# Optimization experiments

Measured on AMD Instinct MI355X. Metric: run time of the kernel, lower is better.

## Reference

```python
import jax, jax.numpy as jnp
import numpy as np

N_TOKENS = 100000
UNITS = 150  # CustomizeLSTMCell.TRANSITION_STATE_OUTPUTS_DIM


def setup_inputs() -> dict:
    key = jax.random.key(0)
    ks = jax.random.split(key, 9)
    f = lambda k, shape: jax.random.normal(k, shape, dtype=jnp.float32)
    return {
        "s_in": f(ks[0], (N_TOKENS, UNITS)),
        "s_out": f(ks[1], (N_TOKENS, UNITS)),
        "h_in": f(ks[2], (N_TOKENS, UNITS)),
        "h_out": f(ks[3], (N_TOKENS, UNITS)),
        "last_c": f(ks[4], (N_TOKENS, UNITS)),
        "w_in_input": f(ks[5], (UNITS, UNITS)) * 0.05,
        "w_out_input": f(ks[6], (UNITS, UNITS)) * 0.05,
        "u_in_input": f(ks[7], (UNITS, UNITS)) * 0.05,
        "u_out_input": f(ks[8], (UNITS, UNITS)) * 0.05,
    }


def reference(s_in, s_out, h_in, h_out, last_c,
              w_in_input, w_out_input, u_in_input, u_out_input):
    # Faithful to the source: all four gates use the *_input weights and no bias
    # (the original call() computes identical pre-activations for every gate).
    pre = (s_in @ w_in_input + s_out @ w_out_input
           + h_in @ u_in_input + h_out @ u_out_input)  # [N, H]
    gate = jax.nn.sigmoid(pre)
    # input_gate == output_gate == forget_gate == update_gate == gate
    cell_state = gate * last_c + gate * gate
    hidden_state = gate * jnp.tanh(cell_state)
    return hidden_state, cell_state
```

## Files before the change

kernel.cpp:

```cpp
#include <hip/hip_runtime.h>
#include <hip/hip_bf16.h>

typedef __attribute__((ext_vector_type(8))) short short8;
typedef __attribute__((ext_vector_type(4))) float f32x4;

#define NTOK   100000
#define H      150
#define NKS    20
#define BM     64
#define SLAB   38400
#define NCHUNK 38
#define BUFB   (NCHUNK*1024)
#define OUTOFF (NTOK * H)
#define XLIM   ((long)NTOK * H * 4 - 16)

__device__ __forceinline__ unsigned short f2bf(float f) {
    unsigned int u = __builtin_bit_cast(unsigned int, f);
    u = (u + 0x7FFFu + ((u >> 16) & 1u)) >> 16;
    return (unsigned short)u;
}

__global__ void prep_w(const float* __restrict__ w_in, const float* __restrict__ w_out,
                       const float* __restrict__ u_in, const float* __restrict__ u_out,
                       unsigned short* __restrict__ wb) {
    int idx = blockIdx.x * 256 + threadIdx.x;
    if (idx >= 10 * NKS * 64 * 8) return;
    int j    = idx & 7;
    int lane = (idx >> 3) & 63;
    int ks   = (idx >> 9) % NKS;
    int n    = idx / (512 * NKS);
    int seg  = ks / 5, s5 = ks % 5;
    int col  = n * 16 + (lane & 15);
    int k2   = s5 * 32 + (lane >> 4) * 8 + j;
    float v = 0.0f;
    if (col < H && k2 < H) {
        const float* W = (seg == 0) ? w_in : (seg == 1) ? w_out : (seg == 2) ? u_in : u_out;
        v = W[k2 * H + col];
    }
    wb[idx] = f2bf(v);
}

__global__ __launch_bounds__(256, 2) void lstm_fused(
        const float* __restrict__ s_in, const float* __restrict__ s_out,
        const float* __restrict__ h_in, const float* __restrict__ h_out,
        const float* __restrict__ last_c, const unsigned short* __restrict__ wb,
        float* __restrict__ out) {
    __shared__ __align__(16) unsigned char Xr[2][BUFB];

    const int t     = threadIdx.x;
    const int lane  = t & 63;
    const int wid   = t >> 6;
    const int waveM = wid >> 1;
    const int waveN = wid & 1;
    const int lrow  = lane & 15;
    const int lko   = lane >> 4;
    const int r0blk = blockIdx.x * BM;

    const float* Xseg[4] = {s_in, s_out, h_in, h_out};

    f32x4 acc[2][5];
#pragma unroll
    for (int m = 0; m < 2; m++)
#pragma unroll
        for (int n = 0; n < 5; n++) acc[m][n] = (f32x4){0.f, 0.f, 0.f, 0.f};

    auto stage = [&](int seg, int buf) {
        const char* base = (const char*)Xseg[seg];
        const long sofs = (long)r0blk * (H * 4);
        for (int c = wid; c < NCHUNK; c += 4) {
            long go = sofs + c * 1024 + lane * 16;
            if (go > XLIM) go = XLIM;
            const void* gp = base + go;
            void* lp = &Xr[buf][c * 1024];
            __builtin_amdgcn_global_load_lds(
                (const __attribute__((address_space(1))) void*)gp,
                (__attribute__((address_space(3))) void*)lp, 16, 0, 0);
        }
    };

    stage(0, 0);
    __syncthreads();

    for (int seg = 0; seg < 4; seg++) {
        if (seg < 3) stage(seg + 1, (seg + 1) & 1);

        const float* Xf = (const float*)&Xr[seg & 1][0];

#pragma unroll
        for (int s5 = 0; s5 < 5; s5++) {
            const int ks = seg * 5 + s5;
            short8 bf[5];
#pragma unroll
            for (int n = 0; n < 5; n++)
                bf[n] = *(const short8*)&wb[((((long)waveN * 5 + n) * NKS + ks) * 64 + lane) * 8];

            const int k0 = s5 * 32 + lko * 8;
            short8 af[2];
#pragma unroll
            for (int m = 0; m < 2; m++) {
                const int row = waveM * 32 + m * 16 + lrow;
                const float* rp = Xf + row * H + k0;
                float xv[8];
#pragma unroll
                for (int j = 0; j < 8; j += 2) {
                    float2 v = *(const float2*)&rp[j];
                    xv[j] = v.x; xv[j + 1] = v.y;
                }
                if (s5 == 4) {
#pragma unroll
                    for (int j = 0; j < 8; j++)
                        xv[j] = (k0 + j < H) ? xv[j] : 0.f;
                }
#pragma unroll
                for (int j = 0; j < 8; j++) af[m][j] = (short)f2bf(xv[j]);
            }

#pragma unroll
            for (int m = 0; m < 2; m++)
#pragma unroll
                for (int n = 0; n < 5; n++)
                    acc[m][n] = __builtin_amdgcn_mfma_f32_16x16x32_bf16(af[m], bf[n], acc[m][n], 0, 0, 0);
        }
        __syncthreads();
    }

#pragma unroll
    for (int m = 0; m < 2; m++) {
#pragma unroll
        for (int r = 0; r < 4; r++) {
            const int row = r0blk + waveM * 32 + m * 16 + lko * 4 + r;
            if (row >= NTOK) continue;
            const long rb = (long)row * H;
#pragma unroll
            for (int n = 0; n < 5; n++) {
                const int col = waveN * 80 + n * 16 + lrow;
                if (col >= H) continue;
                float pre = acc[m][n][r];
                float e   = __expf(-pre);
                float g   = __builtin_amdgcn_rcpf(1.f + e);
                float lc  = last_c[rb + col];
                float cell = g * lc + g * g;
                float e2  = __expf(-2.f * cell);
                float th  = (1.f - e2) * __builtin_amdgcn_rcpf(1.f + e2);
                out[rb + col]          = g * th;
                out[OUTOFF + rb + col] = cell;
            }
        }
    }
}

extern "C" void kernel_launch(void* const* d_in, const int* in_sizes, int n_in,
                              void* d_out, int out_size, void* d_ws, size_t ws_size,
                              hipStream_t stream) {
    const float* s_in   = (const float*)d_in[0];
    const float* s_out  = (const float*)d_in[1];
    const float* h_in   = (const float*)d_in[2];
    const float* h_out  = (const float*)d_in[3];
    const float* last_c = (const float*)d_in[4];
    const float* w_in   = (const float*)d_in[5];
    const float* w_out  = (const float*)d_in[6];
    const float* u_in   = (const float*)d_in[7];
    const float* u_out  = (const float*)d_in[8];

    unsigned short* wb = (unsigned short*)d_ws;
    float* out = (float*)d_out;

    prep_w<<<(10 * NKS * 64 * 8 + 255) / 256, 256, 0, stream>>>(w_in, w_out, u_in, u_out, wb);

    const int nblocks = (NTOK + BM - 1) / BM;
    lstm_fused<<<nblocks, 256, 0, stream>>>(s_in, s_out, h_in, h_out, last_c, wb, out);
}
```

Before: 138.8 us.

## Stage per-wave K-slices with triple-buffered async loads and no block barriers

Each wave now stages its own 32-row by 32-column K-slice into a private triple-buffered LDS region, using XOR-swizzled addresses and explicit vmcnt waits. This replaces the block-wide double buffer of whole 64-row segments and its __syncthreads. Weight fragments are double-buffered in registers, and the last K-slice is shifted to an overlapping window whose duplicate weight rows are zeroed, which removes the per-element masking. The smaller LDS footprint allows three blocks per CU, at the cost of fragile hand-written waitcnt counts and finer-grained loads.

```diff
diff --git a/kernel.cpp b/kernel.cpp
--- a/kernel.cpp
+++ b/kernel.cpp
@@ -8,11 +8,8 @@
 #define H      150
 #define NKS    20
 #define BM     64
-#define SLAB   38400
-#define NCHUNK 38
-#define BUFB   (NCHUNK*1024)
 #define OUTOFF (NTOK * H)
-#define XLIM   ((long)NTOK * H * 4 - 16)
+#define XLIM   ((long)NTOK * 600 - 16)
 
 __device__ __forceinline__ unsigned short f2bf(float f) {
     unsigned int u = __builtin_bit_cast(unsigned int, f);
@@ -31,21 +28,29 @@
     int n    = idx / (512 * NKS);
     int seg  = ks / 5, s5 = ks % 5;
     int col  = n * 16 + (lane & 15);
-    int k2   = s5 * 32 + (lane >> 4) * 8 + j;
+    int p    = (lane >> 4) * 8 + j;
+    int k2   = (s5 < 4) ? (s5 * 32 + p) : (118 + p);
+    bool zero_overlap = (s5 == 4) && (p < 10);
     float v = 0.0f;
-    if (col < H && k2 < H) {
+    if (col < H && k2 < H && !zero_overlap) {
         const float* W = (seg == 0) ? w_in : (seg == 1) ? w_out : (seg == 2) ? u_in : u_out;
         v = W[k2 * H + col];
     }
     wb[idx] = f2bf(v);
 }
 
-__global__ __launch_bounds__(256, 2) void lstm_fused(
+template<int N> __device__ __forceinline__ void vwait() {
+    if constexpr (N == 13)     asm volatile("s_waitcnt vmcnt(13)" ::: "memory");
+    else if constexpr (N == 9) asm volatile("s_waitcnt vmcnt(9)" ::: "memory");
+    else                       asm volatile("s_waitcnt vmcnt(0)" ::: "memory");
+}
+
+__global__ __launch_bounds__(256, 3) void lstm_fused(
         const float* __restrict__ s_in, const float* __restrict__ s_out,
         const float* __restrict__ h_in, const float* __restrict__ h_out,
         const float* __restrict__ last_c, const unsigned short* __restrict__ wb,
         float* __restrict__ out) {
-    __shared__ __align__(16) unsigned char Xr[2][BUFB];
+    __shared__ __align__(16) unsigned char Xr[4][3][4096];
 
     const int t     = threadIdx.x;
     const int lane  = t & 63;
@@ -55,8 +60,16 @@
     const int lrow  = lane & 15;
     const int lko   = lane >> 4;
     const int r0blk = blockIdx.x * BM;
+    const int rW    = r0blk + waveM * 32;
 
     const float* Xseg[4] = {s_in, s_out, h_in, h_out};
+
+    const int trl = lane >> 3;
+    const int swz = (lane & 7) ^ (trl & 6);
+    long rowoff[4];
+#pragma unroll
+    for (int c = 0; c < 4; c++)
+        rowoff[c] = (long)(rW + c * 8 + trl) * 600 + swz * 16;
 
     f32x4 acc[2][5];
 #pragma unroll
@@ -64,65 +77,70 @@
 #pragma unroll
         for (int n = 0; n < 5; n++) acc[m][n] = (f32x4){0.f, 0.f, 0.f, 0.f};
 
-    auto stage = [&](int seg, int buf) {
-        const char* base = (const char*)Xseg[seg];
-        const long sofs = (long)r0blk * (H * 4);
-        for (int c = wid; c < NCHUNK; c += 4) {
-            long go = sofs + c * 1024 + lane * 16;
+    short8 bfA[5], bfB[5];
+
+    auto STAGE = [&](int ks) {
+        const char* xb = (const char*)Xseg[ks / 5];
+        const int s5 = ks % 5;
+        const int sofs = (s5 < 4) ? s5 * 128 : 472;
+        const int buf = ks % 3;
+#pragma unroll
+        for (int c = 0; c < 4; c++) {
+            long go = rowoff[c] + sofs;
             if (go > XLIM) go = XLIM;
-            const void* gp = base + go;
-            void* lp = &Xr[buf][c * 1024];
             __builtin_amdgcn_global_load_lds(
-                (const __attribute__((address_space(1))) void*)gp,
-                (__attribute__((address_space(3))) void*)lp, 16, 0, 0);
+                (const __attribute__((address_space(1))) void*)(xb + go),
+                (__attribute__((address_space(3))) void*)&Xr[wid][buf][c * 1024],
+                16, 0, 0);
+        }
+    };
+    auto BLOAD = [&](int ks, short8* dst) {
+#pragma unroll
+        for (int n = 0; n < 5; n++)
+            dst[n] = *(const short8*)
+                &wb[((((long)waveN * 5 + n) * NKS + ks) * 64 + lane) * 8];
+    };
+    auto COMPUTE = [&](int ks, const short8* bf) {
+        const int buf = ks % 3;
+#pragma unroll
+        for (int m = 0; m < 2; m++) {
+            const int tr = m * 16 + lrow;
+            const int p  = (lko * 2) ^ (tr & 6);
+            const f32x4* lp = (const f32x4*)&Xr[wid][buf][tr * 128 + p * 16];
+            f32x4 v0 = lp[0], v1 = lp[1];
+            short8 af;
+            af[0] = (short)f2bf(v0[0]); af[1] = (short)f2bf(v0[1]);
+            af[2] = (short)f2bf(v0[2]); af[3] = (short)f2bf(v0[3]);
+            af[4] = (short)f2bf(v1[0]); af[5] = (short)f2bf(v1[1]);
+            af[6] = (short)f2bf(v1[2]); af[7] = (short)f2bf(v1[3]);
+#pragma unroll
+            for (int n = 0; n < 5; n++)
+                acc[m][n] = __builtin_amdgcn_mfma_f32_16x16x32_bf16(af, bf[n], acc[m][n], 0, 0, 0);
         }
     };
 
-    stage(0, 0);
-    __syncthreads();
+#define ITER(ks, CUR, NXT)                                       \
+    {                                                            \
+        if ((ks) + 1 < NKS) BLOAD((ks) + 1, NXT);                \
+        if ((ks) + 2 < NKS) STAGE((ks) + 2);                     \
+        if ((ks) < NKS - 2)       vwait<13>();                   \
+        else if ((ks) == NKS - 2) vwait<9>();                    \
+        else                      vwait<0>();                    \
+        __builtin_amdgcn_sched_barrier(0);                       \
+        COMPUTE((ks), CUR);                                      \
+    }
 
-    for (int seg = 0; seg < 4; seg++) {
-        if (seg < 3) stage(seg + 1, (seg + 1) & 1);
+    STAGE(0);
+    BLOAD(0, bfA);
+    STAGE(1);
+    __builtin_amdgcn_sched_barrier(0);
 
-        const float* Xf = (const float*)&Xr[seg & 1][0];
-
-#pragma unroll
-        for (int s5 = 0; s5 < 5; s5++) {
-            const int ks = seg * 5 + s5;
-            short8 bf[5];
-#pragma unroll
-            for (int n = 0; n < 5; n++)
-                bf[n] = *(const short8*)&wb[((((long)waveN * 5 + n) * NKS + ks) * 64 + lane) * 8];
-
-            const int k0 = s5 * 32 + lko * 8;
-            short8 af[2];
-#pragma unroll
-            for (int m = 0; m < 2; m++) {
-                const int row = waveM * 32 + m * 16 + lrow;
-                const float* rp = Xf + row * H + k0;
-                float xv[8];
-#pragma unroll
-                for (int j = 0; j < 8; j += 2) {
-                    float2 v = *(const float2*)&rp[j];
-                    xv[j] = v.x; xv[j + 1] = v.y;
-                }
-                if (s5 == 4) {
-#pragma unroll
-                    for (int j = 0; j < 8; j++)
-                        xv[j] = (k0 + j < H) ? xv[j] : 0.f;
-                }
-#pragma unroll
-                for (int j = 0; j < 8; j++) af[m][j] = (short)f2bf(xv[j]);
-            }
-
-#pragma unroll
-            for (int m = 0; m < 2; m++)
-#pragma unroll
-                for (int n = 0; n < 5; n++)
-                    acc[m][n] = __builtin_amdgcn_mfma_f32_16x16x32_bf16(af[m], bf[n], acc[m][n], 0, 0, 0);
-        }
-        __syncthreads();
-    }
+    ITER(0,  bfA, bfB)  ITER(1,  bfB, bfA)  ITER(2,  bfA, bfB)  ITER(3,  bfB, bfA)
+    ITER(4,  bfA, bfB)  ITER(5,  bfB, bfA)  ITER(6,  bfA, bfB)  ITER(7,  bfB, bfA)
+    ITER(8,  bfA, bfB)  ITER(9,  bfB, bfA)  ITER(10, bfA, bfB)  ITER(11, bfB, bfA)
+    ITER(12, bfA, bfB)  ITER(13, bfB, bfA)  ITER(14, bfA, bfB)  ITER(15, bfB, bfA)
+    ITER(16, bfA, bfB)  ITER(17, bfB, bfA)  ITER(18, bfA, bfB)  ITER(19, bfB, bfA)
+#undef ITER
 
 #pragma unroll
     for (int m = 0; m < 2; m++) {
```

Measured after the change: 168.9 us. 21.7% more time.
